# Performance work log

Measured on AMD Instinct MI355X. Metric: run time of the kernel, lower is better.

Reference implementation:

```python
import jax, jax.numpy as jnp
import numpy as np


def make_coord(h, w, dtype=jnp.float32):
    # grid-center coords in [-1, 1], shape [h, w, 2] with dim0 = row coord, dim1 = col coord
    rh = 1.0 / h
    rw = 1.0 / w
    sh = -1.0 + rh + 2.0 * rh * jnp.arange(h, dtype=dtype)
    sw = -1.0 + rw + 2.0 * rw * jnp.arange(w, dtype=dtype)
    yy, xx = jnp.meshgrid(sh, sw, indexing='ij')
    return jnp.stack([yy, xx], axis=-1)


def nearest_sample(img, gy, gx):
    # img: [B, C, H, W]; gy/gx: [B, N] normalized coords in [-1,1]
    # Replicates F.grid_sample(mode='nearest', align_corners=False, padding_mode='zeros')
    B, C, H, W = img.shape
    fy = (gy + 1.0) * H / 2.0 - 0.5
    fx = (gx + 1.0) * W / 2.0 - 0.5
    iy = jnp.floor(fy + 0.5).astype(jnp.int32)
    ix = jnp.floor(fx + 0.5).astype(jnp.int32)
    valid = (iy >= 0) & (iy < H) & (ix >= 0) & (ix < W)
    iyc = jnp.clip(iy, 0, H - 1)
    ixc = jnp.clip(ix, 0, W - 1)

    def gather_one(im, iy_b, ix_b):
        return im[:, iy_b, ix_b].T  # [N, C]

    out = jax.vmap(gather_one)(img, iyc, ixc)  # [B, N, C]
    return out * valid[..., None].astype(img.dtype)


def mlp(x, w1, b1, w2, b2, w3, b3, w4, b4, w5, b5):
    x = jax.nn.relu(x @ w1 + b1)
    x = jax.nn.relu(x @ w2 + b2)
    x = jax.nn.relu(x @ w3 + b3)
    x = jax.nn.relu(x @ w4 + b4)
    return x @ w5 + b5


def setup_inputs() -> dict:
    key = jax.random.key(0)
    ks = jax.random.split(key, 16)
    B, Cf, h, w = 2, 128, 64, 64
    H, W = 256, 256
    N = H * W
    feat = jax.random.normal(ks[0], (B, Cf, h, w), jnp.float32)
    hr_guide = jax.random.normal(ks[1], (B, 128, H, W), jnp.float32)
    lr_guide = jax.random.normal(ks[2], (B, 128, h, w), jnp.float32)
    coord = jnp.broadcast_to(make_coord(H, W).reshape(1, N, 2), (B, N, 2))
    dims = [386, 1024, 512, 256, 128, 2]
    params = {}
    for i in range(5):
        params['w%d' % (i + 1)] = jax.random.normal(ks[3 + i], (dims[i], dims[i + 1]), jnp.float32) * 0.02
        params['b%d' % (i + 1)] = jnp.zeros((dims[i + 1],), jnp.float32)
    out = {'feat': feat, 'coord': coord, 'hr_guide': hr_guide, 'lr_guide': lr_guide}
    out.update(params)
    return out


def reference(feat, coord, hr_guide, lr_guide, w1, b1, w2, b2, w3, b3, w4, b4, w5, b5):
    B, Cf, h, w = feat.shape
    dt = coord.dtype
    # [B, 2, h, w] coordinate map of low-res grid centers
    feat_coord = jnp.broadcast_to(
        make_coord(h, w, dt).transpose(2, 0, 1)[None], (B, 2, h, w))
    # grid = coord.flip(-1): grid x = coord[...,1] indexes W, grid y = coord[...,0] indexes H
    q_guide_hr = nearest_sample(hr_guide, coord[..., 0], coord[..., 1])  # [B, N, G]
    rx = 1.0 / h
    ry = 1.0 / w
    scale = jnp.array([h, w], dtype=dt)
    preds = []
    for vx in (-1.0, 1.0):
        for vy in (-1.0, 1.0):
            cy = coord[..., 0] + vx * rx
            cx = coord[..., 1] + vy * ry
            q_feat = nearest_sample(feat, cy, cx)          # [B, N, Cf]
            q_coord = nearest_sample(feat_coord, cy, cx)   # [B, N, 2]
            rel_coord = (coord - q_coord) * scale          # [B, N, 2]
            q_guide_lr = nearest_sample(lr_guide, cy, cx)  # [B, N, G]
            q_guide = jnp.concatenate([q_guide_hr, q_guide_hr - q_guide_lr], axis=-1)
            inp = jnp.concatenate([q_feat, q_guide, rel_coord], axis=-1)  # [B, N, 386]
            preds.append(mlp(inp, w1, b1, w2, b2, w3, b3, w4, b4, w5, b5))  # [B, N, 2]
    preds = jnp.stack(preds, axis=-1)                 # [B, N, 2, 4]
    weight = jax.nn.softmax(preds[:, :, 1, :], axis=-1)  # [B, N, 4]
    ret = jnp.sum(preds[:, :, 0, :] * weight, axis=-1, keepdims=True)  # [B, N, 1]
    return ret
```

## Files before the change

### kernel.cpp

```cpp
#include <hip/hip_runtime.h>


typedef unsigned short u16;
typedef unsigned int   u32;
typedef __bf16  bf16x8 __attribute__((ext_vector_type(8)));
typedef float   f32x4  __attribute__((ext_vector_type(4)));
typedef unsigned short u16x8 __attribute__((ext_vector_type(8)));

__device__ __forceinline__ u16 f2bf(float f) {
  __bf16 h = (__bf16)f;
  return __builtin_bit_cast(u16, h);
}
__device__ __forceinline__ float bf2f(u16 v) {
  return __uint_as_float(((u32)v) << 16);
}
__device__ __forceinline__ void gload_lds16(const void* g, void* l) {
  __builtin_amdgcn_global_load_lds(
      (const __attribute__((address_space(1))) void*)g,
      (__attribute__((address_space(3))) void*)l, 16, 0, 0);
}

__global__ __launch_bounds__(256)
void gather_hr(const float* __restrict__ coord, const float* __restrict__ hr,
               u16* __restrict__ Xhr, int* __restrict__ cellidx, float* __restrict__ rel)
{
  __shared__ u16 hrT[64 * 130];
  __shared__ int nhrS[64];

  const int tid = threadIdx.x;
  const int pb  = blockIdx.x << 6;
  const int b   = pb >> 16;
  const int n0  = pb & 65535;
  const float rh = 0.015625f;

  if (tid < 64) {
    const int n = n0 + tid;
    const float cy = coord[(size_t)(b * 65536 + n) * 2 + 0];
    const float cx = coord[(size_t)(b * 65536 + n) * 2 + 1];
    float fyh = (cy + 1.0f) * 128.0f - 0.5f;
    float fxh = (cx + 1.0f) * 128.0f - 0.5f;
    int iyh = (int)floorf(fyh + 0.5f);
    int ixh = (int)floorf(fxh + 0.5f);
    bool vh = (iyh >= 0 && iyh < 256 && ixh >= 0 && ixh < 256);
    nhrS[tid] = vh ? ((iyh << 8) + ixh) : -1;
#pragma unroll
    for (int k = 0; k < 4; ++k) {
      const float vx = (k < 2) ? -1.0f : 1.0f;
      const float vy = (k & 1) ? 1.0f : -1.0f;
      const float cyk = cy + vx * rh;
      const float cxk = cx + vy * rh;
      float fy = (cyk + 1.0f) * 32.0f - 0.5f;
      float fx = (cxk + 1.0f) * 32.0f - 0.5f;
      int iy = (int)floorf(fy + 0.5f);
      int ix = (int)floorf(fx + 0.5f);
      bool valid = (iy >= 0 && iy < 64 && ix >= 0 && ix < 64);
      int iyc = min(max(iy, 0), 63);
      int ixc = min(max(ix, 0), 63);
      float qy = valid ? ((-1.0f + rh) + (2.0f * rh) * (float)iyc) : 0.0f;
      float qx = valid ? ((-1.0f + rh) + (2.0f * rh) * (float)ixc) : 0.0f;
      const int p4 = ((pb + tid) << 2) + k;
      rel[2 * p4 + 0] = (cy - qy) * 64.0f;
      rel[2 * p4 + 1] = (cx - qx) * 64.0f;
      cellidx[p4] = valid ? (b * 4096 + iyc * 64 + ixc) : -1;
    }
  }
  __syncthreads();

  const size_t hb = (size_t)b * 128 * 65536;
  for (int e = tid; e < 64 * 128; e += 256) {
    const int pix = e & 63, c = e >> 6;
    const int n = nhrS[pix];
    const float v = (n >= 0) ? hr[hb + (size_t)c * 65536 + n] : 0.0f;
    hrT[pix * 130 + c] = f2bf(v);
  }
  __syncthreads();

  for (int e = tid; e < 64 * 128; e += 256) {
    const int pix = e >> 7, c = e & 127;
    Xhr[(size_t)(pb + pix) * 128 + c] = hrT[pix * 130 + c];
  }
}

__global__ __launch_bounds__(256)
void prep_cells(const float* __restrict__ feat, const float* __restrict__ lr,
                u16* __restrict__ Xcell)
{
  __shared__ u16 t[64 * 258];
  const int tid = threadIdx.x;
  const int cb = blockIdx.x << 6;
  const int b = cb >> 12;
  const int local = cb & 4095;
  const size_t fb = (size_t)b * 128 * 4096;
  for (int e = tid; e < 64 * 128; e += 256) {
    const int cell = e & 63, c = e >> 6;
    const size_t idx = fb + (size_t)c * 4096 + local + cell;
    t[cell * 258 + c]       = f2bf(feat[idx]);
    t[cell * 258 + 128 + c] = (u16)(f2bf(lr[idx]) ^ 0x8000u);
  }
  __syncthreads();
  for (int e = tid; e < 64 * 256; e += 256) {
    const int cell = e >> 8, c = e & 255;
    Xcell[(size_t)(cb + cell) * 256 + c] = t[cell * 258 + c];
  }
}

template<int MODE>
__global__ __launch_bounds__(256)
void gemm_bt(const u16* __restrict__ A, const u16* __restrict__ BT,
             void* __restrict__ Cout, const float* __restrict__ bias,
             int M, int N, int K)
{
  __shared__ __align__(16) u16 sh[16384];
  u16* As = sh;
  u16* Bs = sh + 8192;

  const int tid = threadIdx.x;
  const int w = tid >> 6;
  const int lane = tid & 63;
  const int ntn = N >> 7;
  const int nmt = M >> 7;
  int bm, bn;
  if ((nmt & 7) == 0) {
    const int xcd = blockIdx.x & 7;
    const int t = blockIdx.x >> 3;
    bn = t % ntn;
    bm = xcd * (nmt >> 3) + t / ntn;
  } else {
    bm = blockIdx.x / ntn;
    bn = blockIdx.x - bm * ntn;
  }
  const int m0 = bm << 7, n0 = bn << 7;

  const int lrow = tid >> 2;
  const int cc   = tid & 3;
  const int gcol = (cc ^ ((lrow >> 1) & 3)) << 3;

  f32x4 acc[4][4];
#pragma unroll
  for (int ii = 0; ii < 4; ++ii)
#pragma unroll
    for (int jj = 0; jj < 4; ++jj)
      acc[ii][jj] = f32x4{0.f, 0.f, 0.f, 0.f};

  const int mbase = (w & 1) << 6;
  const int nbase = (w >> 1) << 6;
  const int fr = lane & 15;
  const int fq = lane >> 4;
  const int rchunk = (fq ^ ((fr >> 1) & 3)) << 3;

  for (int kt = 0; kt < K; kt += 64) {
#pragma unroll
    for (int s = 0; s < 2; ++s) {
      const int kb = kt + (s << 5);
#pragma unroll
      for (int q = 0; q < 2; ++q) {
        const int mrow = (q << 6) + lrow;
        gload_lds16(A + (size_t)(m0 + mrow) * K + (kb + gcol),
                    (char*)As + (s << 13) + (q << 12) + (w << 10));
        gload_lds16(BT + (size_t)(n0 + mrow) * K + (kb + gcol),
                    (char*)Bs + (s << 13) + (q << 12) + (w << 10));
      }
    }
    __syncthreads();
#pragma unroll
    for (int s = 0; s < 2; ++s) {
      const int so = s << 12;
      bf16x8 af[4], bfv[4];
#pragma unroll
      for (int ii = 0; ii < 4; ++ii) {
        af[ii]  = *(const bf16x8*)(As + so + ((mbase + (ii << 4) + fr) << 5) + rchunk);
        bfv[ii] = *(const bf16x8*)(Bs + so + ((nbase + (ii << 4) + fr) << 5) + rchunk);
      }
#pragma unroll
      for (int ii = 0; ii < 4; ++ii)
#pragma unroll
        for (int jj = 0; jj < 4; ++jj)
          acc[ii][jj] = __builtin_amdgcn_mfma_f32_16x16x32_bf16(af[ii], bfv[jj], acc[ii][jj], 0, 0, 0);
    }
    __syncthreads();
  }

#pragma unroll
  for (int jj = 0; jj < 4; ++jj) {
    const int ncol = n0 + nbase + (jj << 4) + fr;
    const float bi = (MODE == 0 || MODE == 1) ? bias[ncol] : 0.f;
#pragma unroll
    for (int ii = 0; ii < 4; ++ii) {
#pragma unroll
      for (int r = 0; r < 4; ++r) {
        const int mrow = m0 + mbase + (ii << 4) + (fq << 2) + r;
        if (MODE == 0) {
          ((u16*)Cout)[(size_t)mrow * N + ncol] = f2bf(fmaxf(acc[ii][jj][r] + bi, 0.f));
        } else if (MODE == 1) {
          ((u16*)Cout)[(size_t)mrow * N + ncol] = f2bf(acc[ii][jj][r] + bi);
        } else {
          ((u16*)Cout)[(size_t)mrow * N + ncol] = f2bf(acc[ii][jj][r]);
        }
      }
    }
  }
}

__global__ __launch_bounds__(512, 2)
void gemm_l12(const u16* __restrict__ Yhr, const u16* __restrict__ Ycell,
              const u16* __restrict__ W1rb, const int* __restrict__ cellidx,
              const float* __restrict__ rel, const u16* __restrict__ BT,
              u16* __restrict__ Cout, const float* __restrict__ bias,
              int M, int K, int gp0)
{
  __shared__ __align__(16) u16 sh[81920];
  char* shb = (char*)sh;
  const int N = 512;

  const int tid  = threadIdx.x;
  const int w    = tid >> 6;
  const int lane = tid & 63;
  const int wm = w >> 2, wn = w & 3;
  const int nwg = M >> 7;
  int bid = blockIdx.x;
  if ((nwg & 7) == 0) {
    const int cpx = nwg >> 3;
    bid = (bid & 7) * cpx + (bid >> 3);
  }
  const int m0 = bid << 7;
  const int NT = K >> 6;

  const int srow = tid >> 3;
  const int cg   = tid & 7;
  const int gk   = (cg ^ (srow & 7)) << 3;
  const int swz8 = gk;

  const int fr = lane & 15;
  const int fq = lane >> 4;
  const int pk0 = ((fq)     ^ (fr & 7)) << 3;
  const int pk1 = ((4 + fq) ^ (fr & 7)) << 3;
  const int awr = (wm << 6) + fr;
  const int bwr = (wn << 7) + fr;

  const int m04 = m0 >> 2;
  const int kk  = srow & 3;
  const int pA  = m04 + (srow >> 2);
  const int pB  = pA + 16;
  const int idxA = (gp0 + pA) * 4 + kk;
  const int idxB = (gp0 + pB) * 4 + kk;
  const int cellA = cellidx[idxA];
  const int cellB = cellidx[idxB];
  const float2 rvA = *(const float2*)(rel + (size_t)idxA * 2);
  const float2 rvB = *(const float2*)(rel + (size_t)idxB * 2);
  const float ryA = rvA.x, rxA = rvA.y, ryB = rvB.x, rxB = rvB.y;
  const u16 mkA = (u16)(cellA >= 0 ? 0xFFFFu : 0u);
  const u16 mkB = (u16)(cellB >= 0 ? 0xFFFFu : 0u);
  const u16x8 mskA = {mkA, mkA, mkA, mkA, mkA, mkA, mkA, mkA};
  const u16x8 mskB = {mkB, mkB, mkB, mkB, mkB, mkB, mkB, mkB};
  const u16* yA = Yhr + (size_t)pA * 1024;
  const u16* yB = Yhr + (size_t)pB * 1024;
  const u16* zA = Ycell + (size_t)max(cellA, 0) * 1024;
  const u16* zB = Ycell + (size_t)max(cellB, 0) * 1024;

  u16x8 yhA, yhB, ycA, ycB, cw0, cw1;

#define A_LOADS(kt1_) do { const int co_ = (kt1_) + (cg << 3); \
    yhA = *(const u16x8*)(yA + co_); yhB = *(const u16x8*)(yB + co_); \
    ycA = *(const u16x8*)(zA + co_); ycB = *(const u16x8*)(zB + co_); \
    cw0 = *(const u16x8*)(W1rb + co_); cw1 = *(const u16x8*)(W1rb + 1024 + co_); } while (0)

#define A_CONS(ab_) do { \
    const u16x8 za_ = ycA & mskA, zb_ = ycB & mskB; \
    u16x8 oA_, oB_; \
    _Pragma("unroll") \
    for (int j_ = 0; j_ < 8; ++j_) { \
      const float f0_ = bf2f(cw0[j_]), f1_ = bf2f(cw1[j_]); \
      float vA_ = bf2f(yhA[j_]) + bf2f(za_[j_]) + ryA * f0_ + rxA * f1_; \
      float vB_ = bf2f(yhB[j_]) + bf2f(zb_[j_]) + ryB * f0_ + rxB * f1_; \
      oA_[j_] = f2bf(fmaxf(vA_, 0.f)); \
      oB_[j_] = f2bf(fmaxf(vB_, 0.f)); \
    } \
    *(u16x8*)(sh + (ab_) + (srow << 6) + swz8) = oA_; \
    *(u16x8*)(sh + (ab_) + ((64 + srow) << 6) + swz8) = oB_; } while (0)

#define STAGE_B(q_, kt_) do { \
    _Pragma("unroll") \
    for (int h_ = 0; h_ < 8; ++h_) \
      gload_lds16(BT + (size_t)((h_ << 6) + srow) * K + (kt_) + gk, \
                  shb + 32768 + ((q_) << 16) + (h_ << 13) + (w << 10)); } while (0)
#define BAR12()   asm volatile("s_barrier" ::: "memory")
#define VMC(n)    asm volatile("s_waitcnt vmcnt(" #n ")" ::: "memory")
#define LGKM0_()  asm volatile("s_waitcnt lgkmcnt(0)" ::: "memory")

  f32x4 acc[4][8];
#pragma unroll
  for (int i = 0; i < 4; ++i)
#pragma unroll
    for (int j = 0; j < 8; ++j)
      acc[i][j] = f32x4{0.f, 0.f, 0.f, 0.f};

  A_LOADS(0);
  A_CONS(0);
  STAGE_B(0, 0);
  if (NT > 1) { A_LOADS(64); VMC(6); }
  else VMC(0);
  LGKM0_();
  BAR12();

  for (int t = 0; t < NT; ++t) {
    const int Ab = (t & 1) << 13;
    const int Bb = 16384 + ((t & 1) << 15);
    const int p1 = (t + 1) & 1;
    const int kt1 = (t + 1) << 6;
    const bool mA_ = (t + 1 < NT);
    const bool mG_ = (t + 2 < NT);

    bf16x8 a0[4], g0[8];
#pragma unroll
    for (int i = 0; i < 4; ++i)
      a0[i] = *(const bf16x8*)(sh + Ab + ((awr + (i << 4)) << 6) + pk0);
#pragma unroll
    for (int j = 0; j < 8; ++j)
      g0[j] = *(const bf16x8*)(sh + Bb + ((bwr + (j << 4)) << 6) + pk0);
    if (mA_) STAGE_B(p1, kt1);
    __builtin_amdgcn_s_setprio(1);
#pragma unroll
    for (int i = 0; i < 4; ++i)
#pragma unroll
      for (int j = 0; j < 8; ++j)
        acc[i][j] = __builtin_amdgcn_mfma_f32_16x16x32_bf16(a0[i], g0[j], acc[i][j], 0, 0, 0);
    __builtin_amdgcn_s_setprio(0);
    if (mA_) A_CONS(p1 << 13);

    bf16x8 a1[4], g1[8];
#pragma unroll
    for (int i = 0; i < 4; ++i)
      a1[i] = *(const bf16x8*)(sh + Ab + ((awr + (i << 4)) << 6) + pk1);
#pragma unroll
    for (int j = 0; j < 8; ++j)
      g1[j] = *(const bf16x8*)(sh + Bb + ((bwr + (j << 4)) << 6) + pk1);
    if (mG_) A_LOADS((t + 2) << 6);
    if (mG_) VMC(6); else VMC(0);
    LGKM0_();
    BAR12();
    __builtin_amdgcn_s_setprio(1);
#pragma unroll
    for (int i = 0; i < 4; ++i)
#pragma unroll
      for (int j = 0; j < 8; ++j)
        acc[i][j] = __builtin_amdgcn_mfma_f32_16x16x32_bf16(a1[i], g1[j], acc[i][j], 0, 0, 0);
    __builtin_amdgcn_s_setprio(0);
  }

#undef A_LOADS
#undef A_CONS
#undef STAGE_B
#undef BAR12
#undef VMC
#undef LGKM0_

#pragma unroll
  for (int j = 0; j < 8; ++j) {
    const int ncol = (wn << 7) + (j << 4) + fr;
    const float bi = bias[ncol];
#pragma unroll
    for (int i = 0; i < 4; ++i) {
#pragma unroll
      for (int r = 0; r < 4; ++r) {
        const int mrow = m0 + (wm << 6) + (i << 4) + (fq << 2) + r;
        Cout[(size_t)mrow * N + ncol] = f2bf(fmaxf(acc[i][j][r] + bi, 0.f));
      }
    }
  }
}

__global__ __launch_bounds__(512, 4)
void tail34(const u16* __restrict__ A2, const u16* __restrict__ W3T,
            const u16* __restrict__ W4T, const float* __restrict__ b3,
            const float* __restrict__ b4, const float* __restrict__ w5,
            const float* __restrict__ b5, float* __restrict__ outp,
            int M, int gp0)
{
  __shared__ __align__(16) u16 sh[40960];
  u16* As  = sh;
  u16* Bs  = sh + 8192;
  u16* A3s = sh;
  u16* W4s = sh + 32768;

  const int tid = threadIdx.x;
  const int w = tid >> 6;
  const int lane = tid & 63;
  const int wm = w >> 2, wn = w & 3;
  const int nmt = M >> 7;
  int bm;
  if ((nmt & 7) == 0) bm = (blockIdx.x & 7) * (nmt >> 3) + (blockIdx.x >> 3);
  else bm = blockIdx.x;
  const int m0 = bm << 7;

  const int lrow = tid >> 2;
  const int cc   = tid & 3;
  const int gcol = (cc ^ ((lrow >> 1) & 3)) << 3;

  const int fr = lane & 15;
  const int fq = lane >> 4;
  const int rchunk = (fq ^ ((fr >> 1) & 3)) << 3;
  const int nb3 = wn << 6;

  f32x4 acc3[4][4];
#pragma unroll
  for (int ii = 0; ii < 4; ++ii)
#pragma unroll
    for (int jj = 0; jj < 4; ++jj)
      acc3[ii][jj] = f32x4{0.f, 0.f, 0.f, 0.f};

  for (int kt = 0; kt < 512; kt += 64) {
#pragma unroll
    for (int s = 0; s < 2; ++s) {
      const int kb = kt + (s << 5);
      gload_lds16(A2 + (size_t)(m0 + lrow) * 512 + (kb + gcol),
                  (char*)As + (s << 13) + (w << 10));
#pragma unroll
      for (int q = 0; q < 2; ++q) {
        gload_lds16(W3T + (size_t)((q << 7) + lrow) * 512 + (kb + gcol),
                    (char*)Bs + (s << 14) + (q << 13) + (w << 10));
      }
    }
    __syncthreads();
#pragma unroll
    for (int s = 0; s < 2; ++s) {
      bf16x8 af[4], bfv[4];
#pragma unroll
      for (int ii = 0; ii < 4; ++ii) {
        af[ii]  = *(const bf16x8*)(As + (s << 12) + (((wm << 6) + (ii << 4) + fr) << 5) + rchunk);
        bfv[ii] = *(const bf16x8*)(Bs + (s << 13) + ((nb3 + (ii << 4) + fr) << 5) + rchunk);
      }
#pragma unroll
      for (int ii = 0; ii < 4; ++ii)
#pragma unroll
        for (int jj = 0; jj < 4; ++jj)
          acc3[ii][jj] = __builtin_amdgcn_mfma_f32_16x16x32_bf16(af[ii], bfv[jj], acc3[ii][jj], 0, 0, 0);
    }
    __syncthreads();
  }

  float b3v[4];
#pragma unroll
  for (int jj = 0; jj < 4; ++jj) b3v[jj] = b3[nb3 + (jj << 4) + fr];
#pragma unroll
  for (int jj = 0; jj < 4; ++jj) {
    const int col = nb3 + (jj << 4) + fr;
    const int sl = col >> 5, c = col & 31;
#pragma unroll
    for (int ii = 0; ii < 4; ++ii) {
#pragma unroll
      for (int r = 0; r < 4; ++r) {
        const int row = (wm << 6) + (ii << 4) + (fq << 2) + r;
        A3s[(sl << 12) + (row << 5) + (((c >> 3) ^ ((row >> 1) & 3)) << 3) + (c & 7)] =
            f2bf(fmaxf(acc3[ii][jj][r] + b3v[jj], 0.f));
      }
    }
  }

  f32x4 acc4[4][2];
#pragma unroll
  for (int ii = 0; ii < 4; ++ii)
#pragma unroll
    for (int jj = 0; jj < 2; ++jj)
      acc4[ii][jj] = f32x4{0.f, 0.f, 0.f, 0.f};
  const int nb4 = wn << 5;

  for (int kt4 = 0; kt4 < 4; ++kt4) {
#pragma unroll
    for (int s = 0; s < 2; ++s) {
      const int kb = (kt4 << 6) + (s << 5);
      gload_lds16(W4T + (size_t)lrow * 256 + (kb + gcol),
                  (char*)W4s + (s << 13) + (w << 10));
    }
    __syncthreads();
#pragma unroll
    for (int s = 0; s < 2; ++s) {
      const int sl = (kt4 << 1) + s;
      bf16x8 af[4], bfv[2];
#pragma unroll
      for (int ii = 0; ii < 4; ++ii)
        af[ii] = *(const bf16x8*)(A3s + (sl << 12) + (((wm << 6) + (ii << 4) + fr) << 5) + rchunk);
#pragma unroll
      for (int jj = 0; jj < 2; ++jj)
        bfv[jj] = *(const bf16x8*)(W4s + (s << 12) + ((nb4 + (jj << 4) + fr) << 5) + rchunk);
#pragma unroll
      for (int ii = 0; ii < 4; ++ii)
#pragma unroll
        for (int jj = 0; jj < 2; ++jj)
          acc4[ii][jj] = __builtin_amdgcn_mfma_f32_16x16x32_bf16(af[ii], bfv[jj], acc4[ii][jj], 0, 0, 0);
    }
    __syncthreads();
  }

  float b4v[2];
#pragma unroll
  for (int jj = 0; jj < 2; ++jj) b4v[jj] = b4[nb4 + (jj << 4) + fr];
#pragma unroll
  for (int ii = 0; ii < 4; ++ii) {
#pragma unroll
    for (int jj = 0; jj < 2; ++jj) {
      const int col = nb4 + (jj << 4) + fr;
#pragma unroll
      for (int r = 0; r < 4; ++r) {
        const int row = (wm << 6) + (ii << 4) + (fq << 2) + r;
        sh[row * 136 + col] = f2bf(fmaxf(acc4[ii][jj][r] + b4v[jj], 0.f));
      }
    }
  }
  const int cbase = fr << 3;
  float w50[8], w51[8];
#pragma unroll
  for (int j = 0; j < 8; ++j) {
    w50[j] = w5[((cbase + j) << 1) + 0];
    w51[j] = w5[((cbase + j) << 1) + 1];
  }
  const float b50 = b5[0], b51 = b5[1];
  __syncthreads();

#pragma unroll
  for (int rep = 0; rep < 4; ++rep) {
    const int pl = (rep << 3) + w;
    const int row = (pl << 2) + fq;
    const u16x8 v = *(const u16x8*)(sh + row * 136 + cbase);
    float s0 = 0.f, s1 = 0.f;
#pragma unroll
    for (int j = 0; j < 8; ++j) {
      const float a = bf2f(v[j]);
      s0 += a * w50[j];
      s1 += a * w51[j];
    }
#pragma unroll
    for (int off = 8; off >= 1; off >>= 1) {
      s0 += __shfl_xor(s0, off, 16);
      s1 += __shfl_xor(s1, off, 16);
    }
    float p0[4], p1[4];
#pragma unroll
    for (int k = 0; k < 4; ++k) {
      p0[k] = __shfl(s0, k << 4, 64) + b50;
      p1[k] = __shfl(s1, k << 4, 64) + b51;
    }
    if (lane == 0) {
      float mx = fmaxf(fmaxf(p1[0], p1[1]), fmaxf(p1[2], p1[3]));
      float e0 = expf(p1[0] - mx), e1 = expf(p1[1] - mx);
      float e2 = expf(p1[2] - mx), e3 = expf(p1[3] - mx);
      outp[gp0 + (m0 >> 2) + pl] =
          (p0[0] * e0 + p0[1] * e1 + p0[2] * e2 + p0[3] * e3) / (e0 + e1 + e2 + e3);
    }
  }
}

__global__ __launch_bounds__(256)
void prep_all(const float* __restrict__ w1, const float* __restrict__ w2,
              const float* __restrict__ w3, const float* __restrict__ w4,
              u16* __restrict__ W1hrT, u16* __restrict__ W1cellT,
              u16* __restrict__ W2T, u16* __restrict__ W3T, u16* __restrict__ W4T,
              u16* __restrict__ W1rb)
{
  const int idx = blockIdx.x * 256 + threadIdx.x;
  if (idx < 131072) {
    const int n = idx >> 7, k = idx & 127;
    W1hrT[idx] = f2bf(w1[(128 + k) * 1024 + n] + w1[(256 + k) * 1024 + n]);
  } else if (idx < 393216) {
    const int i = idx - 131072;
    const int n = i >> 8, k = i & 255;
    W1cellT[i] = f2bf((k < 128) ? w1[k * 1024 + n] : w1[(128 + k) * 1024 + n]);
  } else if (idx < 917504) {
    const int i = idx - 393216;
    const int n = i >> 10, k = i & 1023;
    W2T[i] = f2bf(w2[k * 512 + n]);
  } else if (idx < 1048576) {
    const int i = idx - 917504;
    const int n = i >> 9, k = i & 511;
    W3T[i] = f2bf(w3[k * 256 + n]);
  } else if (idx < 1081344) {
    const int i = idx - 1048576;
    const int n = i >> 8, k = i & 255;
    W4T[i] = f2bf(w4[k * 128 + n]);
  } else if (idx < 1083392) {
    const int i = idx - 1081344;
    W1rb[i] = f2bf(w1[384 * 1024 + i]);
  }
}

extern "C" void kernel_launch(void* const* d_in, const int* in_sizes, int n_in,
                              void* d_out, int out_size, void* d_ws, size_t ws_size,
                              hipStream_t stream)
{
  const float* feat  = (const float*)d_in[0];
  const float* coord = (const float*)d_in[1];
  const float* hrg   = (const float*)d_in[2];
  const float* lrg   = (const float*)d_in[3];
  const float* w1 = (const float*)d_in[4];
  const float* b1 = (const float*)d_in[5];
  const float* w2 = (const float*)d_in[6];
  const float* b2 = (const float*)d_in[7];
  const float* w3 = (const float*)d_in[8];
  const float* b3 = (const float*)d_in[9];
  const float* w4 = (const float*)d_in[10];
  const float* b4 = (const float*)d_in[11];
  const float* w5 = (const float*)d_in[12];
  const float* b5 = (const float*)d_in[13];
  float* out = (float*)d_out;

  char* base = (char*)d_ws;
  u16* W1hrT   = (u16*)base;
  u16* W1cellT = W1hrT + 1024 * 128;
  u16* W2T     = W1cellT + 1024 * 256;
  u16* W3T     = W2T + 512 * 1024;
  u16* W4T     = W3T + 256 * 512;
  u16* W1rb    = W4T + 128 * 256;
  u16* Xcell   = W1rb + 2048;
  u16* Ycell   = Xcell + 8192 * 256;
  u16* Xhr     = Ycell + (size_t)8192 * 1024;
  float* relb  = (float*)(Xhr + (size_t)131072 * 128);
  int* cellidx = (int*)(relb + (size_t)131072 * 8);
  char* chunk_base = (char*)(cellidx + (size_t)131072 * 4);
  const size_t fixed = (size_t)(chunk_base - base);

  const int NP = 131072;
  int nc = 1;
  while (nc < 128 && fixed + (size_t)(NP / nc) * 6144ULL > ws_size) nc <<= 1;
  const int CP = NP / nc;
  const int R = CP * 4;

  u16* Yhr = (u16*)chunk_base;
  u16* A2  = Yhr + (size_t)CP * 1024;

  prep_all<<<4232, 256, 0, stream>>>(w1, w2, w3, w4, W1hrT, W1cellT, W2T, W3T,
                                     W4T, W1rb);
  gather_hr<<<NP / 64, 256, 0, stream>>>(coord, hrg, Xhr, cellidx, relb);
  prep_cells<<<8192 / 64, 256, 0, stream>>>(feat, lrg, Xcell);
  gemm_bt<3><<<(8192 / 128) * (1024 / 128), 256, 0, stream>>>(
      Xcell, W1cellT, (void*)Ycell, nullptr, 8192, 1024, 256);

  for (int ch = 0; ch < nc; ++ch) {
    const int gp0 = ch * CP;
    gemm_bt<1><<<(CP / 128) * (1024 / 128), 256, 0, stream>>>(
        Xhr + (size_t)gp0 * 128, W1hrT, (void*)Yhr, b1, CP, 1024, 128);
    gemm_l12<<<(R >> 7), 512, 0, stream>>>(
        Yhr, Ycell, W1rb, cellidx, relb, W2T, A2, b2, R, 1024, gp0);
    tail34<<<R / 128, 512, 0, stream>>>(
        A2, W3T, W4T, b3, b4, w5, b5, out, R, gp0);
  }
}
```

Measured before the change: 1.093 ms.

## Fuse layer-2 GEMM with layers 3-5 tail, keeping activations in LDS

Merges the layer-2 GEMM kernel and the layer-3/4/5 tail kernel into one. The ReLU'd layer-2 output tile (128x512 bf16) now goes to swizzled shared memory and is read directly as the A operand of the layer-3 GEMM, so the A2 round trip through global memory is gone. Workspace per chunk shrinks, which can allow fewer chunks. The cost is that the fused kernel runs at the gemm_l12 occupancy (launch bounds 2) rather than the tail's 4, and it has a longer serial body with a larger LDS footprint.

Measured after the change: 1.018 ms. 1.07x faster.

```diff
diff --git a/kernel.cpp b/kernel.cpp
--- a/kernel.cpp
+++ b/kernel.cpp
@@ -202,15 +202,17 @@
 }
 
 __global__ __launch_bounds__(512, 2)
-void gemm_l12(const u16* __restrict__ Yhr, const u16* __restrict__ Ycell,
-              const u16* __restrict__ W1rb, const int* __restrict__ cellidx,
-              const float* __restrict__ rel, const u16* __restrict__ BT,
-              u16* __restrict__ Cout, const float* __restrict__ bias,
-              int M, int K, int gp0)
+void gemm_l12t(const u16* __restrict__ Yhr, const u16* __restrict__ Ycell,
+               const u16* __restrict__ W1rb, const int* __restrict__ cellidx,
+               const float* __restrict__ rel, const u16* __restrict__ BT,
+               const float* __restrict__ bias, const u16* __restrict__ W3T,
+               const u16* __restrict__ W4T, const float* __restrict__ b3,
+               const float* __restrict__ b4, const float* __restrict__ w5,
+               const float* __restrict__ b5, float* __restrict__ outp,
+               int M, int K, int gp0)
 {
   __shared__ __align__(16) u16 sh[81920];
   char* shb = (char*)sh;
-  const int N = 512;
 
   const int tid  = threadIdx.x;
   const int w    = tid >> 6;
@@ -358,48 +360,26 @@
   for (int j = 0; j < 8; ++j) {
     const int ncol = (wn << 7) + (j << 4) + fr;
     const float bi = bias[ncol];
+    const int chnk = ncol >> 3, sub = ncol & 7;
 #pragma unroll
     for (int i = 0; i < 4; ++i) {
 #pragma unroll
       for (int r = 0; r < 4; ++r) {
-        const int mrow = m0 + (wm << 6) + (i << 4) + (fq << 2) + r;
-        Cout[(size_t)mrow * N + ncol] = f2bf(fmaxf(acc[i][j][r] + bi, 0.f));
-      }
-    }
-  }
-}
-
-__global__ __launch_bounds__(512, 4)
-void tail34(const u16* __restrict__ A2, const u16* __restrict__ W3T,
-            const u16* __restrict__ W4T, const float* __restrict__ b3,
-            const float* __restrict__ b4, const float* __restrict__ w5,
-            const float* __restrict__ b5, float* __restrict__ outp,
-            int M, int gp0)
-{
-  __shared__ __align__(16) u16 sh[40960];
-  u16* As  = sh;
-  u16* Bs  = sh + 8192;
-  u16* A3s = sh;
-  u16* W4s = sh + 32768;
-
-  const int tid = threadIdx.x;
-  const int w = tid >> 6;
-  const int lane = tid & 63;
-  const int wm = w >> 2, wn = w & 3;
-  const int nmt = M >> 7;
-  int bm;
-  if ((nmt & 7) == 0) bm = (blockIdx.x & 7) * (nmt >> 3) + (blockIdx.x >> 3);
-  else bm = blockIdx.x;
-  const int m0 = bm << 7;
+        const int row = (wm << 6) + (i << 4) + (fq << 2) + r;
+        sh[row * 512 + (((chnk ^ (row & 7)) << 3) | sub)] =
+            f2bf(fmaxf(acc[i][j][r] + bi, 0.f));
+      }
+    }
+  }
 
   const int lrow = tid >> 2;
   const int cc   = tid & 3;
   const int gcol = (cc ^ ((lrow >> 1) & 3)) << 3;
-
-  const int fr = lane & 15;
-  const int fq = lane >> 4;
   const int rchunk = (fq ^ ((fr >> 1) & 3)) << 3;
   const int nb3 = wn << 6;
+  u16* W3s = sh + 65536;
+  u16* A3s = sh;
+  u16* W4s = sh + 65536;
 
   f32x4 acc3[4][4];
 #pragma unroll
@@ -412,22 +392,23 @@
 #pragma unroll
     for (int s = 0; s < 2; ++s) {
       const int kb = kt + (s << 5);
-      gload_lds16(A2 + (size_t)(m0 + lrow) * 512 + (kb + gcol),
-                  (char*)As + (s << 13) + (w << 10));
 #pragma unroll
       for (int q = 0; q < 2; ++q) {
         gload_lds16(W3T + (size_t)((q << 7) + lrow) * 512 + (kb + gcol),
-                    (char*)Bs + (s << 14) + (q << 13) + (w << 10));
+                    (char*)W3s + (s << 14) + (q << 13) + (w << 10));
       }
     }
     __syncthreads();
 #pragma unroll
     for (int s = 0; s < 2; ++s) {
+      const int kb = kt + (s << 5);
       bf16x8 af[4], bfv[4];
 #pragma unroll
       for (int ii = 0; ii < 4; ++ii) {
-        af[ii]  = *(const bf16x8*)(As + (s << 12) + (((wm << 6) + (ii << 4) + fr) << 5) + rchunk);
-        bfv[ii] = *(const bf16x8*)(Bs + (s << 13) + ((nb3 + (ii << 4) + fr) << 5) + rchunk);
+        const int row = (wm << 6) + (ii << 4) + fr;
+        af[ii] = *(const bf16x8*)(sh + row * 512 +
+                                  ((((kb >> 3) + fq) ^ (row & 7)) << 3));
+        bfv[ii] = *(const bf16x8*)(W3s + (s << 13) + ((nb3 + (ii << 4) + fr) << 5) + rchunk);
       }
 #pragma unroll
       for (int ii = 0; ii < 4; ++ii)
@@ -619,12 +600,11 @@
 
   const int NP = 131072;
   int nc = 1;
-  while (nc < 128 && fixed + (size_t)(NP / nc) * 6144ULL > ws_size) nc <<= 1;
+  while (nc < 128 && fixed + (size_t)(NP / nc) * 2048ULL > ws_size) nc <<= 1;
   const int CP = NP / nc;
   const int R = CP * 4;
 
   u16* Yhr = (u16*)chunk_base;
-  u16* A2  = Yhr + (size_t)CP * 1024;
 
   prep_all<<<4232, 256, 0, stream>>>(w1, w2, w3, w4, W1hrT, W1cellT, W2T, W3T,
                                      W4T, W1rb);
@@ -637,9 +617,8 @@
     const int gp0 = ch * CP;
     gemm_bt<1><<<(CP / 128) * (1024 / 128), 256, 0, stream>>>(
         Xhr + (size_t)gp0 * 128, W1hrT, (void*)Yhr, b1, CP, 1024, 128);
-    gemm_l12<<<(R >> 7), 512, 0, stream>>>(
-        Yhr, Ycell, W1rb, cellidx, relb, W2T, A2, b2, R, 1024, gp0);
-    tail34<<<R / 128, 512, 0, stream>>>(
-        A2, W3T, W4T, b3, b4, w5, b5, out, R, gp0);
-  }
-}
+    gemm_l12t<<<(R >> 7), 512, 0, stream>>>(
+        Yhr, Ycell, W1rb, cellidx, relb, W2T, b2, W3T, W4T, b3, b4, w5, b5,
+        out, R, 1024, gp0);
+  }
+}
```
